# Kernel optimization log

Measured on AMD Instinct MI355X. Metric: run time of the kernel, lower is better.

## Reference

```python
import jax, jax.numpy as jnp
import numpy as np
from jax import lax

PI = jnp.pi
KX = jnp.array([[-1, 0, 1], [-2, 0, 2], [-1, 0, 1]], jnp.float32)
KY = jnp.array([[-1, -2, -1], [0, 0, 0], [1, 2, 1]], jnp.float32)
K45 = jnp.array([[-2, -1, 0], [-1, 0, 1], [0, 1, 2]], jnp.float32)
K135 = jnp.array([[0, 1, 2], [-1, 0, 1], [-2, -1, 0]], jnp.float32)


def _shift(x, dx, dy):
    # result[i, j] = x[clip(i - dx), clip(j - dy)]  (replicate boundary),
    # exactly matching the torch slice + replicate-pad neighbor construction.
    H, W = x.shape[2], x.shape[3]
    ri = jnp.clip(jnp.arange(H) - dx, 0, H - 1)
    ci = jnp.clip(jnp.arange(W) - dy, 0, W - 1)
    return x[:, :, ri[:, None], ci[None, :]]


def _adaptive_smoothing(f, k=10.0, iter_num=3):
    neighbors = [(-1, -1), (-1, 0), (-1, 1), (0, -1), (0, 0), (0, 1), (1, -1), (1, 0), (1, 1)]
    for _ in range(iter_num):
        Gx = (_shift(f, -1, 0) - _shift(f, 1, 0)) * 0.5   # gradient along H
        Gy = (_shift(f, 0, -1) - _shift(f, 0, 1)) * 0.5   # gradient along W
        w = jnp.exp(-(Gx * Gx + Gy * Gy) / (2.0 * k * k))
        f_new = jnp.zeros_like(f)
        w_sum = jnp.zeros_like(f)
        for dx, dy in neighbors:
            f_new = f_new + _shift(f, dx, dy) * _shift(w, dx, dy)
            w_sum = w_sum + _shift(w, dx, dy)
        f = f_new / jnp.maximum(w_sum, 1e-8)
    return f


def _dwconv(x, k2d):
    # depthwise 3x3 cross-correlation, zero padding (torch Conv2d semantics)
    C = x.shape[1]
    kern = jnp.broadcast_to(k2d[None, None], (C, 1, 3, 3)).astype(x.dtype)
    return lax.conv_general_dilated(x, kern, (1, 1), ((1, 1), (1, 1)),
                                    dimension_numbers=('NCHW', 'OIHW', 'NCHW'),
                                    feature_group_count=C)


def _sobel(x):
    return 0.5 * jnp.abs(_dwconv(x, KX)) + 0.5 * jnp.abs(_dwconv(x, KY))


def _hardswish(x):
    return x * jnp.clip(x + 3.0, 0.0, 6.0) / 6.0


def _canny(data, sigma, weight):
    blurred = _adaptive_smoothing(data, k=10.0, iter_num=3)
    sob = _sobel(blurred)
    B, C, H, W = sob.shape
    # torch.median: lower median = sorted[(n-1)//2]; .item() detaches it
    flat = jnp.sort(sob.reshape(B, C, H * W), axis=-1)
    med = lax.stop_gradient(jnp.mean(flat[:, :, (H * W - 1) // 2]))
    low = jnp.clip((1.0 - sigma) * med, 0.001, 1.0)
    high = jnp.clip((1.0 + sigma) * med, 0.001, 1.0)

    ex = _dwconv(blurred, KX)
    ey = _dwconv(blurred, KY)
    e45 = _dwconv(blurred, K45)
    e135 = _dwconv(blurred, K135)
    mag = jnp.sqrt(ex * ex + ey * ey + e45 * e45 + e135 * e135)
    ang = jnp.mod(jnp.arctan2(ey, ex), PI)

    dirs = jnp.array([0.0, PI / 4, PI / 2, 3 * PI / 4], jnp.float32)
    d = jnp.abs(ang[..., None] - dirs)
    dir_w = jax.nn.softmax(-jnp.minimum(d, PI - d) / 0.01, axis=-1)  # (B,C,H,W,4)

    pm = jnp.pad(mag, ((0, 0), (0, 0), (1, 1), (1, 1)), mode='edge')
    neigh = [(pm[:, :, 1:-1, :-2], pm[:, :, 1:-1, 2:]),
             (pm[:, :, :-2, :-2], pm[:, :, 2:, 2:]),
             (pm[:, :, :-2, 1:-1], pm[:, :, 2:, 1:-1]),
             (pm[:, :, :-2, 2:], pm[:, :, 2:, :-2])]
    sup = jnp.zeros_like(mag)
    for i, (n1, n2) in enumerate(neigh):  # fixed 4-direction loop
        sw = jax.nn.softmax(jnp.stack([mag, n1, n2], axis=-1) / 0.1, axis=-1)[..., 0]
        sup = sup + mag * sw * dir_w[..., i]

    mx = jnp.max(sup)
    sup = sup / jnp.where(mx > 0, mx, 1.0)

    Sh = _hardswish(sup - high)
    Sl = _hardswish(sup - low)
    ecanny = sup * (Sh + Sl)
    dilated = _dwconv(Sh, jnp.ones((3, 3), jnp.float32))
    result = ecanny + dilated * Sl * (1.0 - Sh)

    # enhance_edges with the ORIGINAL input
    result = (1.0 - weight) * result + weight * _sobel(data)
    rmin = jnp.min(result)
    rmax = jnp.max(result)
    return (result - rmin) / (rmax - rmin)


def setup_inputs() -> dict:
    key = jax.random.key(0)
    k1, k2 = jax.random.split(key)
    B, C, H, W = 8, 1, 512, 512
    return {
        'img1': jax.random.uniform(k1, (B, C, H, W), dtype=jnp.float32),
        'img2': jax.random.uniform(k2, (B, C, H, W), dtype=jnp.float32),
        'sigma1': jnp.float32(2.2),
        'enhance_weight1': jnp.float32(0.0),
        'sigma2': jnp.float32(2.2),
        'enhance_weight2': jnp.float32(0.0),
    }


def reference(img1, img2, sigma1, enhance_weight1, sigma2, enhance_weight2):
    s1 = 1.0 - jax.nn.sigmoid(sigma1)
    w1 = jax.nn.sigmoid(enhance_weight1)
    s2 = 1.0 - jax.nn.sigmoid(sigma2)
    w2 = jax.nn.sigmoid(enhance_weight2)
    m1 = _canny(img1, s1, w1)
    m2 = _canny(img2, s2, w2)
    f = (1.0 - m1) * (1.0 - m2) + m1 * m2
    return (1.0 - f, m1, m2)
```

## Files before the change

### kernel.cpp

```cpp
#include <hip/hip_runtime.h>

namespace {

constexpr int H = 512;
constexpr int W = 512;
constexpr int HW = H * W;
constexpr int PPS = 8;
constexpr int NP = 16;
constexpr int TX = 64;
constexpr int TY = 16;
constexpr int STY = 16;
constexpr int NBLK = (W / TX) * (H / TY) * NP;
constexpr float PI_F = 3.14159265358979323846f;
constexpr int NBINS = 1024;
constexpr float BIN_SCALE = 512.0f;

__device__ __forceinline__ float hsw(float x) {
    float t = fminf(fmaxf(x + 3.0f, 0.0f), 6.0f);
    return x * t * (1.0f / 6.0f);
}

__device__ __forceinline__ const float* plane_ptr(const float* s1, const float* s2, int p) {
    return (p < PPS) ? (s1 + (size_t)p * HW) : (s2 + (size_t)(p - PPS) * HW);
}

__device__ __forceinline__ float wave_max(float v) {
    for (int o = 32; o > 0; o >>= 1) v = fmaxf(v, __shfl_down(v, o, 64));
    return v;
}
__device__ __forceinline__ float wave_min(float v) {
    for (int o = 32; o > 0; o >>= 1) v = fminf(v, __shfl_down(v, o, 64));
    return v;
}

__device__ __forceinline__ float atan_poly(float t) {
    float z = t * t;
    float p = -0.01172120f;
    p = p * z + 0.05265332f;
    p = p * z - 0.11643287f;
    p = p * z + 0.19354346f;
    p = p * z - 0.33262347f;
    p = p * z + 0.99997726f;
    return t * p;
}

__device__ __forceinline__ float sel4(int idx, float v0, float v1, float v2, float v3) {
    float a = (idx & 1) ? v1 : v0;
    float b = (idx & 1) ? v3 : v2;
    return (idx & 2) ? b : a;
}

__global__ void K_init(unsigned* hist) {
    int t = blockIdx.x * 256 + threadIdx.x;
    for (int i = t; i < NP * NBINS; i += gridDim.x * 256) hist[i] = 0;
}

__global__ void K_smooth(const float* __restrict__ s1, const float* __restrict__ s2,
                         float* __restrict__ fout) {
    int p = blockIdx.z;
    const float* f = plane_ptr(s1, s2, p);
    int j0 = blockIdx.x * 64, i0 = blockIdx.y * STY;
    __shared__ float fs[STY + 4][68];
    __shared__ float ws[STY + 2][66];
    int tid = threadIdx.y * 64 + threadIdx.x;

    for (int e = tid; e < (STY + 4) * 68; e += 256) {
        int y = e / 68, x = e % 68;
        int gi = min(max(i0 - 2 + y, 0), H - 1);
        int gj = min(max(j0 - 2 + x, 0), W - 1);
        fs[y][x] = f[gi * W + gj];
    }
    __syncthreads();

    for (int e = tid; e < (STY + 2) * 66; e += 256) {
        int y = e / 66, x = e % 66;
        int r = min(max(i0 - 1 + y, 0), H - 1);
        int c = min(max(j0 - 1 + x, 0), W - 1);
        int yr = r - (i0 - 2), xc = c - (j0 - 2);
        int ym = max(r - 1, 0) - (i0 - 2), yp = min(r + 1, H - 1) - (i0 - 2);
        int xm = max(c - 1, 0) - (j0 - 2), xp = min(c + 1, W - 1) - (j0 - 2);
        float gx = 0.5f * (fs[yp][xc] - fs[ym][xc]);
        float gy = 0.5f * (fs[yr][xp] - fs[yr][xm]);
        ws[y][x] = __expf(-(gx * gx + gy * gy) * (1.0f / 200.0f));
    }
    __syncthreads();

    int yl = threadIdx.y * 4;
    int xl = threadIdx.x;
    float rn[6], rd[6];
#pragma unroll
    for (int k = 0; k < 6; k++) {
        float w0 = ws[yl + k][xl], w1 = ws[yl + k][xl + 1], w2 = ws[yl + k][xl + 2];
        float fA = fs[yl + k + 1][xl + 1], fB = fs[yl + k + 1][xl + 2], fC = fs[yl + k + 1][xl + 3];
        rn[k] = fA * w0 + fB * w1 + fC * w2;
        rd[k] = w0 + w1 + w2;
    }
    size_t base = (size_t)p * HW + (i0 + yl) * W + (j0 + xl);
#pragma unroll
    for (int k = 0; k < 4; k++) {
        fout[base + (size_t)k * W] =
            (rn[k] + rn[k + 1] + rn[k + 2]) / fmaxf(rd[k] + rd[k + 1] + rd[k + 2], 1e-8f);
    }
}

__global__ void K_dnms(const float* __restrict__ blur, float* __restrict__ sup,
                       unsigned* __restrict__ hist, float* __restrict__ pmax) {
    int p = blockIdx.z;
    const float* f = blur + (size_t)p * HW;
    int j0 = blockIdx.x * TX, i0 = blockIdx.y * TY;
    __shared__ float fs0[TY + 4][TX + 4];
    __shared__ float ms[TY + 2][TX + 2];
    __shared__ float exs[TY][TX], eys[TY][TX];
    __shared__ unsigned histS[NBINS];
    __shared__ float wred[4];
    int tid = threadIdx.y * 64 + threadIdx.x;

    for (int e = tid; e < NBINS; e += 256) histS[e] = 0;
    for (int e = tid; e < (TY + 4) * (TX + 4); e += 256) {
        int y = e / (TX + 4), x = e % (TX + 4);
        int gi = i0 - 2 + y, gj = j0 - 2 + x;
        fs0[y][x] = (gi >= 0 && gi < H && gj >= 0 && gj < W) ? f[gi * W + gj] : 0.0f;
    }
    __syncthreads();

    for (int e = tid; e < (TY + 2) * (TX + 2); e += 256) {
        int y = e / (TX + 2), x = e % (TX + 2);
        int r = min(max(i0 - 1 + y, 0), H - 1);
        int c = min(max(j0 - 1 + x, 0), W - 1);
        int rr = r - i0 + 2, cc = c - j0 + 2;
        float xmm = fs0[rr - 1][cc - 1], xm0 = fs0[rr - 1][cc], xmp = fs0[rr - 1][cc + 1];
        float x0m = fs0[rr][cc - 1], x0p = fs0[rr][cc + 1];
        float xpm = fs0[rr + 1][cc - 1], xp0 = fs0[rr + 1][cc], xpp = fs0[rr + 1][cc + 1];
        float ex = (xmp - xmm) + 2.0f * (x0p - x0m) + (xpp - xpm);
        float ey = (xpm + 2.0f * xp0 + xpp) - (xmm + 2.0f * xm0 + xmp);
        float e45 = -2.0f * xmm - xm0 - x0m + x0p + xp0 + 2.0f * xpp;
        float e135 = xm0 + 2.0f * xmp - x0m + x0p - 2.0f * xpm - xp0;
        ms[y][x] = sqrtf(ex * ex + ey * ey + e45 * e45 + e135 * e135);
        if (y >= 1 && y <= TY && x >= 1 && x <= TX) {
            exs[y - 1][x - 1] = ex;
            eys[y - 1][x - 1] = ey;
        }
    }
    __syncthreads();

    float bmax = 0.0f;
#pragma unroll
    for (int q = 0; q < TY / 4; q++) {
        int yl = threadIdx.y + q * 4;
        int xl = threadIdx.x;
        float ex = exs[yl][xl], ey = eys[yl][xl];

        float ax = fabsf(ex), ay = fabsf(ey);
        float mn = fminf(ax, ay), mxv = fmaxf(ax, ay);
        float tq = (mxv > 0.0f) ? __fdividef(mn, mxv) : 0.0f;
        float pang = atan_poly(tq);
        if (ay > ax) pang = 1.57079632679f - pang;
        bool obtuse = ((__float_as_uint(ex) ^ __float_as_uint(ey)) & 0x80000000u) != 0u;
        float a = obtuse ? PI_F - pang : pang;

        float fa = a * 1.27323954474f;
        float nf = floorf(fa + 0.5f);
        float diff = a - nf * 0.78539816340f;
        float delta = fabsf(diff);
        int n = (int)nf & 3;
        int m = ((diff >= 0.0f) ? (int)nf + 1 : (int)nf - 1) & 3;
        float t = __expf(200.0f * delta - 78.5398163397f);
        float u = __fdividef(1.0f, 1.0f + t);

        float m0 = ms[yl + 1][xl + 1];
        float n1a = ms[yl + 1][xl], n1b = ms[yl][xl], n1c = ms[yl][xl + 1], n1d = ms[yl][xl + 2];
        float n2a = ms[yl + 1][xl + 2], n2b = ms[yl + 2][xl + 2], n2c = ms[yl + 2][xl + 1], n2d = ms[yl + 2][xl];
        float n1n = sel4(n, n1a, n1b, n1c, n1d);
        float n2n = sel4(n, n2a, n2b, n2c, n2d);
        float n1m = sel4(m, n1a, n1b, n1c, n1d);
        float n2m = sel4(m, n2a, n2b, n2c, n2d);

        float g1n = __expf((n1n - m0) * 10.0f);
        float g2n = __expf((n2n - m0) * 10.0f);
        float g1m = __expf((n1m - m0) * 10.0f);
        float g2m = __expf((n2m - m0) * 10.0f);
        float swn = __fdividef(1.0f, 1.0f + g1n + g2n);
        float swm = __fdividef(1.0f, 1.0f + g1m + g2m);
        float s = m0 * u * (swn + t * swm);

        sup[(size_t)p * HW + (i0 + yl) * W + (j0 + xl)] = s;
        bmax = fmaxf(bmax, s);

        float sv = 0.5f * (ax + ay);
        int bin = min((int)(sv * BIN_SCALE), NBINS - 1);
        atomicAdd(&histS[bin], 1u);
    }

    float wv = wave_max(bmax);
    if ((tid & 63) == 0) wred[tid >> 6] = wv;
    __syncthreads();
    if (tid == 0) {
        int bflat = (blockIdx.z * gridDim.y + blockIdx.y) * gridDim.x + blockIdx.x;
        pmax[bflat] = fmaxf(fmaxf(wred[0], wred[1]), fmaxf(wred[2], wred[3]));
    }
    for (int e = tid; e < NBINS; e += 256)
        if (histS[e]) atomicAdd(&hist[p * NBINS + e], histS[e]);
}

__global__ void K_stats(const unsigned* __restrict__ hist, const float* __restrict__ pmax,
                        float* __restrict__ medv, float* __restrict__ mx) {
    int b = blockIdx.x;
    int t = threadIdx.x;
    if (b < NP) {
        __shared__ unsigned sums[256];
        const unsigned* hp = hist + b * NBINS;
        unsigned s = 0;
        for (int q = 0; q < NBINS / 256; q++) s += hp[t * (NBINS / 256) + q];
        sums[t] = s;
        __syncthreads();
        for (int off = 1; off < 256; off <<= 1) {
            unsigned v = (t >= off) ? sums[t - off] : 0u;
            __syncthreads();
            sums[t] += v;
            __syncthreads();
        }
        const int k = (HW - 1) / 2;
        unsigned base = (t == 0) ? 0u : sums[t - 1];
        if ((int)base <= k && k < (int)sums[t]) {
            int cum = (int)base;
            int bin = t * (NBINS / 256);
            for (int q = 0; q < NBINS / 256; q++) {
                int c = (int)hp[t * (NBINS / 256) + q];
                if (cum + c > k) { bin = t * (NBINS / 256) + q; break; }
                cum += c;
            }
            medv[b] = ((float)bin + 0.5f) * (1.0f / BIN_SCALE);
        }
    } else {
        __shared__ float red[256];
        int s = b - NP;
        const float* base = pmax + s * (NBLK / 2);
        float v = -1e30f;
        for (int i = t; i < NBLK / 2; i += 256) v = fmaxf(v, base[i]);
        red[t] = v;
        __syncthreads();
        for (int sft = 128; sft > 0; sft >>= 1) {
            if (t < sft) red[t] = fmaxf(red[t], red[t + sft]);
            __syncthreads();
        }
        if (t == 0) mx[s] = red[0];
    }
}

__global__ void K_result(const float* __restrict__ sup, const float* __restrict__ im1,
                         const float* __restrict__ im2, const float* __restrict__ medv,
                         const float* __restrict__ sg1, const float* __restrict__ ew1,
                         const float* __restrict__ sg2, const float* __restrict__ ew2,
                         const float* __restrict__ mx, float* __restrict__ res,
                         float* __restrict__ prmax, float* __restrict__ prmin) {
    int p = blockIdx.z;
    int s = p >> 3;
    float med = 0.125f * (medv[s * PPS + 0] + medv[s * PPS + 1] + medv[s * PPS + 2] +
                          medv[s * PPS + 3] + medv[s * PPS + 4] + medv[s * PPS + 5] +
                          medv[s * PPS + 6] + medv[s * PPS + 7]);
    float sgin = (s == 0) ? sg1[0] : sg2[0];
    float ewin = (s == 0) ? ew1[0] : ew2[0];
    float sig = 1.0f - 1.0f / (1.0f + __expf(-sgin));
    float lo = fminf(fmaxf((1.0f - sig) * med, 0.001f), 1.0f);
    float hi = fminf(fmaxf((1.0f + sig) * med, 0.001f), 1.0f);
    float wg = 1.0f / (1.0f + __expf(-ewin));
    float m = mx[s];
    float inv = 1.0f / ((m > 0.0f) ? m : 1.0f);

    const float* sp = sup + (size_t)p * HW;
    const float* op = plane_ptr(im1, im2, p);
    int j0 = blockIdx.x * TX, i0 = blockIdx.y * TY;
    __shared__ float hs2[TY + 2][TX + 2];
    __shared__ float ssn[TY][TX];
    __shared__ float og[TY + 2][TX + 2];
    __shared__ float wredx[4], wredn[4];
    int tid = threadIdx.y * 64 + threadIdx.x;

    for (int e = tid; e < (TY + 2) * (TX + 2); e += 256) {
        int y = e / (TX + 2), x = e % (TX + 2);
        int gi = i0 - 1 + y, gj = j0 - 1 + x;
        float h = 0.0f, o = 0.0f;
        if (gi >= 0 && gi < H && gj >= 0 && gj < W) {
            float sv = sp[gi * W + gj] * inv;
            h = hsw(sv - hi);
            o = op[gi * W + gj];
            if (y >= 1 && y <= TY && x >= 1 && x <= TX) ssn[y - 1][x - 1] = sv;
        }
        hs2[y][x] = h;
        og[y][x] = o;
    }
    __syncthreads();

    int yl = threadIdx.y * 4;
    int xl = threadIdx.x;
    float hrow[6], ddr[6], ssr[6];
#pragma unroll
    for (int k = 0; k < 6; k++) {
        float a = hs2[yl + k][xl], bq = hs2[yl + k][xl + 1], c = hs2[yl + k][xl + 2];
        hrow[k] = a + bq + c;
        float oa = og[yl + k][xl], ob = og[yl + k][xl + 1], oc = og[yl + k][xl + 2];
        ddr[k] = oc - oa;
        ssr[k] = oa + 2.0f * ob + oc;
    }

    float bmx = -1e30f, bmn = 1e30f;
    size_t gbase = (size_t)p * HW + (i0 + yl) * W + (j0 + xl);
#pragma unroll
    for (int k = 0; k < 4; k++) {
        float sn = ssn[yl + k][xl];
        float Sh = hs2[yl + k + 1][xl + 1];
        float Sl = hsw(sn - lo);
        float dil = hrow[k] + hrow[k + 1] + hrow[k + 2];
        float pre = sn * (Sh + Sl) + dil * Sl * (1.0f - Sh);
        float sob = 0.5f * fabsf(ddr[k] + 2.0f * ddr[k + 1] + ddr[k + 2]) +
                    0.5f * fabsf(ssr[k + 2] - ssr[k]);
        float r = (1.0f - wg) * pre + wg * sob;
        res[gbase + (size_t)k * W] = r;
        bmx = fmaxf(bmx, r);
        bmn = fminf(bmn, r);
    }

    float vx = wave_max(bmx), vn = wave_min(bmn);
    if ((tid & 63) == 0) { wredx[tid >> 6] = vx; wredn[tid >> 6] = vn; }
    __syncthreads();
    if (tid == 0) {
        int bflat = (blockIdx.z * gridDim.y + blockIdx.y) * gridDim.x + blockIdx.x;
        prmax[bflat] = fmaxf(fmaxf(wredx[0], wredx[1]), fmaxf(wredx[2], wredx[3]));
        prmin[bflat] = fminf(fminf(wredn[0], wredn[1]), fminf(wredn[2], wredn[3]));
    }
}

__global__ void K_redminmax(const float* __restrict__ prmax, const float* __restrict__ prmin,
                            float* __restrict__ rmaxv, float* __restrict__ rminv) {
    __shared__ float rmx[256], rmn[256];
    int t = threadIdx.x;
    for (int s = 0; s < 2; s++) {
        const float* bx = prmax + s * (NBLK / 2);
        const float* bn = prmin + s * (NBLK / 2);
        float vx = -1e30f, vn = 1e30f;
        for (int i = t; i < NBLK / 2; i += 256) {
            vx = fmaxf(vx, bx[i]);
            vn = fminf(vn, bn[i]);
        }
        rmx[t] = vx;
        rmn[t] = vn;
        __syncthreads();
        for (int sft = 128; sft > 0; sft >>= 1) {
            if (t < sft) {
                rmx[t] = fmaxf(rmx[t], rmx[t + sft]);
                rmn[t] = fminf(rmn[t], rmn[t + sft]);
            }
            __syncthreads();
        }
        if (t == 0) { rmaxv[s] = rmx[0]; rminv[s] = rmn[0]; }
        __syncthreads();
    }
}

__global__ void K_final(const float* __restrict__ res, const float* __restrict__ rmaxv,
                        const float* __restrict__ rminv, float* __restrict__ out) {
    int j = blockIdx.x * 64 + threadIdx.x;
    int i = blockIdx.y * 4 + threadIdx.y;
    int p = blockIdx.z;
    float mx1 = rmaxv[0], mn1 = rminv[0];
    float mx2 = rmaxv[1], mn2 = rminv[1];
    size_t idx = (size_t)p * HW + i * W + j;
    float r1 = res[idx];
    float r2 = res[(size_t)(p + PPS) * HW + i * W + j];
    float m1 = (r1 - mn1) / (mx1 - mn1);
    float m2 = (r2 - mn2) / (mx2 - mn2);
    out[idx] = m1 + m2 - 2.0f * m1 * m2;
    out[(size_t)PPS * HW + idx] = m1;
    out[(size_t)2 * PPS * HW + idx] = m2;
}

}

extern "C" void kernel_launch(void* const* d_in, const int* in_sizes, int n_in,
                              void* d_out, int out_size, void* d_ws, size_t ws_size,
                              hipStream_t stream) {
    const float* img1 = (const float*)d_in[0];
    const float* img2 = (const float*)d_in[1];
    const float* sg1 = (const float*)d_in[2];
    const float* ew1 = (const float*)d_in[3];
    const float* sg2 = (const float*)d_in[4];
    const float* ew2 = (const float*)d_in[5];
    float* out = (float*)d_out;

    float* A = (float*)d_ws;
    float* B = A + (size_t)NP * HW;
    float* C = B + (size_t)NP * HW;
    unsigned* hist = (unsigned*)(C + (size_t)NP * HW);
    float* medv = (float*)(hist + NP * NBINS);
    float* mx = medv + NP;
    float* rmaxv = mx + 2;
    float* rminv = rmaxv + 2;
    float* pmax = rminv + 2;
    float* prmax = pmax + NBLK;
    float* prmin = prmax + NBLK;

    dim3 blk(64, 4, 1);
    dim3 grdT(W / TX, H / TY, NP);
    dim3 grdS(W / 64, H / STY, NP);
    dim3 grdF(W / 64, H / 4, PPS);
    dim3 mblk(256, 1, 1);

    K_init<<<dim3(16), mblk, 0, stream>>>(hist);

    K_smooth<<<grdS, blk, 0, stream>>>(img1, img2, A);
    K_smooth<<<grdS, blk, 0, stream>>>(A, A + (size_t)PPS * HW, B);
    K_smooth<<<grdS, blk, 0, stream>>>(B, B + (size_t)PPS * HW, A);

    K_dnms<<<grdT, blk, 0, stream>>>(A, C, hist, pmax);

    K_stats<<<dim3(NP + 2), mblk, 0, stream>>>(hist, pmax, medv, mx);

    K_result<<<grdT, blk, 0, stream>>>(C, img1, img2, medv, sg1, ew1, sg2, ew2, mx,
                                       B, prmax, prmin);
    K_redminmax<<<dim3(1), mblk, 0, stream>>>(prmax, prmin, rmaxv, rminv);
    K_final<<<grdF, blk, 0, stream>>>(B, rmaxv, rminv, out);
}
```

Baseline: 130.4 us.

## Fold histogram init into smooth kernel and register-tile DNMS stencil per thread

Drops the separate histogram-zeroing kernel launch and clears the histogram inside the first smoothing pass instead. In the DNMS kernel each thread now computes four vertically adjacent pixels from a register cache of the blurred tile. It keeps ex/ey in registers instead of shared arrays, and only the halo ring of the magnitude tile is computed by a subset of threads. This cuts shared-memory traffic, shared memory footprint and one launch, but raises register pressure.

Measured after the change: 120.0 us. 7.9% less time.

```diff
diff --git a/kernel.cpp b/kernel.cpp
--- a/kernel.cpp
+++ b/kernel.cpp
@@ -50,19 +50,18 @@
     return (idx & 2) ? b : a;
 }
 
-__global__ void K_init(unsigned* hist) {
-    int t = blockIdx.x * 256 + threadIdx.x;
-    for (int i = t; i < NP * NBINS; i += gridDim.x * 256) hist[i] = 0;
-}
-
 __global__ void K_smooth(const float* __restrict__ s1, const float* __restrict__ s2,
-                         float* __restrict__ fout) {
+                         float* __restrict__ fout, unsigned* __restrict__ hist) {
+    int tid = threadIdx.y * 64 + threadIdx.x;
+    if (hist) {
+        int bid = (blockIdx.z * gridDim.y + blockIdx.y) * gridDim.x + blockIdx.x;
+        if (bid < (NP * NBINS) / 256) hist[bid * 256 + tid] = 0;
+    }
     int p = blockIdx.z;
     const float* f = plane_ptr(s1, s2, p);
     int j0 = blockIdx.x * 64, i0 = blockIdx.y * STY;
     __shared__ float fs[STY + 4][68];
     __shared__ float ws[STY + 2][66];
-    int tid = threadIdx.y * 64 + threadIdx.x;
 
     for (int e = tid; e < (STY + 4) * 68; e += 256) {
         int y = e / 68, x = e % 68;
@@ -110,7 +109,6 @@
     int j0 = blockIdx.x * TX, i0 = blockIdx.y * TY;
     __shared__ float fs0[TY + 4][TX + 4];
     __shared__ float ms[TY + 2][TX + 2];
-    __shared__ float exs[TY][TX], eys[TY][TX];
     __shared__ unsigned histS[NBINS];
     __shared__ float wred[4];
     int tid = threadIdx.y * 64 + threadIdx.x;
@@ -123,8 +121,37 @@
     }
     __syncthreads();
 
-    for (int e = tid; e < (TY + 2) * (TX + 2); e += 256) {
-        int y = e / (TX + 2), x = e % (TX + 2);
+    int xl = threadIdx.x;
+    int yb = threadIdx.y * 4;
+
+    float fv[6][3];
+#pragma unroll
+    for (int rr = 0; rr < 6; rr++)
+#pragma unroll
+        for (int cc = 0; cc < 3; cc++)
+            fv[rr][cc] = fs0[yb + 1 + rr][xl + 1 + cc];
+
+    float exk[4], eyk[4];
+#pragma unroll
+    for (int k = 0; k < 4; k++) {
+        float xmm = fv[k][0], xm0 = fv[k][1], xmp = fv[k][2];
+        float x0m = fv[k + 1][0], x0p = fv[k + 1][2];
+        float xpm = fv[k + 2][0], xp0 = fv[k + 2][1], xpp = fv[k + 2][2];
+        float ex = (xmp - xmm) + 2.0f * (x0p - x0m) + (xpp - xpm);
+        float ey = (xpm + 2.0f * xp0 + xpp) - (xmm + 2.0f * xm0 + xmp);
+        float e45 = -2.0f * xmm - xm0 - x0m + x0p + xp0 + 2.0f * xpp;
+        float e135 = xm0 + 2.0f * xmp - x0m + x0p - 2.0f * xpm - xp0;
+        ms[yb + 1 + k][xl + 1] = sqrtf(ex * ex + ey * ey + e45 * e45 + e135 * e135);
+        exk[k] = ex;
+        eyk[k] = ey;
+    }
+
+    if (tid < 2 * (TX + 2) + 2 * TY) {
+        int y, x;
+        if (tid < TX + 2) { y = 0; x = tid; }
+        else if (tid < 2 * (TX + 2)) { y = TY + 1; x = tid - (TX + 2); }
+        else if (tid < 2 * (TX + 2) + TY) { y = tid - 2 * (TX + 2) + 1; x = 0; }
+        else { y = tid - (2 * (TX + 2) + TY) + 1; x = TX + 1; }
         int r = min(max(i0 - 1 + y, 0), H - 1);
         int c = min(max(j0 - 1 + x, 0), W - 1);
         int rr = r - i0 + 2, cc = c - j0 + 2;
@@ -136,19 +163,20 @@
         float e45 = -2.0f * xmm - xm0 - x0m + x0p + xp0 + 2.0f * xpp;
         float e135 = xm0 + 2.0f * xmp - x0m + x0p - 2.0f * xpm - xp0;
         ms[y][x] = sqrtf(ex * ex + ey * ey + e45 * e45 + e135 * e135);
-        if (y >= 1 && y <= TY && x >= 1 && x <= TX) {
-            exs[y - 1][x - 1] = ex;
-            eys[y - 1][x - 1] = ey;
-        }
-    }
-    __syncthreads();
+    }
+    __syncthreads();
+
+    float msr[6][3];
+#pragma unroll
+    for (int rr = 0; rr < 6; rr++)
+#pragma unroll
+        for (int cc = 0; cc < 3; cc++)
+            msr[rr][cc] = ms[yb + rr][xl + cc];
 
     float bmax = 0.0f;
 #pragma unroll
-    for (int q = 0; q < TY / 4; q++) {
-        int yl = threadIdx.y + q * 4;
-        int xl = threadIdx.x;
-        float ex = exs[yl][xl], ey = eys[yl][xl];
+    for (int k = 0; k < 4; k++) {
+        float ex = exk[k], ey = eyk[k];
 
         float ax = fabsf(ex), ay = fabsf(ey);
         float mn = fminf(ax, ay), mxv = fmaxf(ax, ay);
@@ -167,9 +195,9 @@
         float t = __expf(200.0f * delta - 78.5398163397f);
         float u = __fdividef(1.0f, 1.0f + t);
 
-        float m0 = ms[yl + 1][xl + 1];
-        float n1a = ms[yl + 1][xl], n1b = ms[yl][xl], n1c = ms[yl][xl + 1], n1d = ms[yl][xl + 2];
-        float n2a = ms[yl + 1][xl + 2], n2b = ms[yl + 2][xl + 2], n2c = ms[yl + 2][xl + 1], n2d = ms[yl + 2][xl];
+        float m0 = msr[k + 1][1];
+        float n1a = msr[k + 1][0], n1b = msr[k][0], n1c = msr[k][1], n1d = msr[k][2];
+        float n2a = msr[k + 1][2], n2b = msr[k + 2][2], n2c = msr[k + 2][1], n2d = msr[k + 2][0];
         float n1n = sel4(n, n1a, n1b, n1c, n1d);
         float n2n = sel4(n, n2a, n2b, n2c, n2d);
         float n1m = sel4(m, n1a, n1b, n1c, n1d);
@@ -183,7 +211,7 @@
         float swm = __fdividef(1.0f, 1.0f + g1m + g2m);
         float s = m0 * u * (swn + t * swm);
 
-        sup[(size_t)p * HW + (i0 + yl) * W + (j0 + xl)] = s;
+        sup[(size_t)p * HW + (i0 + yb + k) * W + (j0 + xl)] = s;
         bmax = fmaxf(bmax, s);
 
         float sv = 0.5f * (ax + ay);
@@ -405,11 +433,9 @@
     dim3 grdF(W / 64, H / 4, PPS);
     dim3 mblk(256, 1, 1);
 
-    K_init<<<dim3(16), mblk, 0, stream>>>(hist);
-
-    K_smooth<<<grdS, blk, 0, stream>>>(img1, img2, A);
-    K_smooth<<<grdS, blk, 0, stream>>>(A, A + (size_t)PPS * HW, B);
-    K_smooth<<<grdS, blk, 0, stream>>>(B, B + (size_t)PPS * HW, A);
+    K_smooth<<<grdS, blk, 0, stream>>>(img1, img2, A, hist);
+    K_smooth<<<grdS, blk, 0, stream>>>(A, A + (size_t)PPS * HW, B, nullptr);
+    K_smooth<<<grdS, blk, 0, stream>>>(B, B + (size_t)PPS * HW, A, nullptr);
 
     K_dnms<<<grdT, blk, 0, stream>>>(A, C, hist, pmax);
 
```
